# Optimization experiments

Measured on AMD Instinct MI355X. Metric: run time of the kernel, lower is better.

The kernel has to match this reference:

```python
import jax, jax.numpy as jnp
import numpy as np

# B trajectories, L spline knots, D data channels, H hidden, W MLP width, OUT outputs
B, L, D, H, W, OUT = 1024, 200, 32, 64, 128, 16
N_STEPS = 100  # dt0 = (ts[-1]-ts[0]) / 100 in the source -> fixed-step Heun over the span


def _mlp3(x, W1, b1, W2, b2, W3, b3, act, final_act=None):
    h = act(x @ W1.T + b1)
    h = act(h @ W2.T + b2)
    o = h @ W3.T + b3
    return final_act(o) if final_act is not None else o


def setup_inputs() -> dict:
    key = jax.random.key(0)
    ks = jax.random.split(key, 16)
    f32 = jnp.float32

    def rn(k, shape, scale):
        return jax.random.normal(k, shape, f32) * scale

    def lin(kk, out_d, in_d):
        kw, kb = jax.random.split(kk)
        s = 1.0 / float(np.sqrt(in_d))
        return rn(kw, (out_d, in_d), s), rn(kb, (out_d,), s)

    inp = {"ts": jnp.arange(L, dtype=f32)}
    for i, n in enumerate(["coef_d", "coef_c", "coef_b", "coef_a"]):
        inp[n] = rn(ks[i], (B, L - 1, D), 0.1)
    inp["iW1"], inp["ib1"] = lin(ks[4], W, D)
    inp["iW2"], inp["ib2"] = lin(ks[5], W, W)
    inp["iW3"], inp["ib3"] = lin(ks[6], H, W)
    inp["fW1"], inp["fb1"] = lin(ks[7], W, H)
    inp["fW2"], inp["fb2"] = lin(ks[8], W, W)
    inp["fW3"], inp["fb3"] = lin(ks[9], H * D, W)
    inp["dW1"], inp["db1"] = lin(ks[10], 128, H)
    inp["dW2"], inp["db2"] = lin(ks[11], 128, 128)
    inp["dW3"], inp["db3"] = lin(ks[12], OUT, 128)
    return inp


def reference(ts, coef_d, coef_c, coef_b, coef_a,
              iW1, ib1, iW2, ib2, iW3, ib3,
              fW1, fb1, fW2, fb2, fW3, fb3,
              dW1, db1, dW2, db2, dW3, db3):
    sp = jax.nn.softplus
    # X(t0) = a[:, 0] (cubic-spline eval at left knot has frac = 0)
    y0 = _mlp3(coef_a[:, 0], iW1, ib1, iW2, ib2, iW3, ib3, sp, final_act=sp)  # [B, H]
    t0 = ts[0]
    dt = (ts[-1] - t0) / N_STEPS

    def dXdt(t):  # cubic spline derivative at scalar time t -> [B, D]
        i = jnp.clip(jnp.searchsorted(ts, t, side="right") - 1, 0, L - 2)
        frac = t - ts[i]
        return coef_b[:, i] + frac * (2.0 * coef_c[:, i] + 3.0 * frac * coef_d[:, i])

    def vf(t, y):  # ControlTerm(func, control).to_ode(): f(y) @ dX/dt
        f = _mlp3(y, fW1, fb1, fW2, fb2, fW3, fb3, sp).reshape(B, H, D)
        return jnp.einsum("bhd,bd->bh", f, dXdt(t))

    def heun_step(y, k):
        t = t0 + k * dt
        k1 = vf(t, y)
        k2 = vf(t + dt, y + dt * k1)
        return y + 0.5 * dt * (k1 + k2), None

    yT, _ = jax.lax.scan(heun_step, y0, jnp.arange(N_STEPS, dtype=ts.dtype))
    # decoder: Linear->relu->Linear->relu->Linear
    return _mlp3(yT, dW1, db1, dW2, db2, dW3, db3, jax.nn.relu)  # [B, OUT]
```

## Files before the change

### kernel.cpp

```cpp
#include <hip/hip_runtime.h>

#define NT 512
#define TRAJ 4

constexpr int Lk = 200;
constexpr int NSTEPS = 100;

__device__ __forceinline__ float sp_act(float x) {
    return fmaxf(x, 0.0f) + log1pf(expf(-fabsf(x)));
}

__global__ void fw3_transpose(const float* __restrict__ w, float* __restrict__ wT) {
    int idx = blockIdx.x * 256 + threadIdx.x;
    int k = idx >> 11;
    int n = idx & 2047;
    wT[idx] = w[n * 128 + k];
}

template<int O, int I>
__device__ __forceinline__ void stage_T(const float* __restrict__ g, float* __restrict__ T) {
    for (int base = threadIdx.x * 4; base < O * I; base += NT * 4) {
        const float4 w = *(const float4*)(g + base);
        const int o = base / I;
        const int i = base % I;
        T[(i + 0) * O + o] = w.x;
        T[(i + 1) * O + o] = w.y;
        T[(i + 2) * O + o] = w.z;
        T[(i + 3) * O + o] = w.w;
    }
}

template<int I, int O, int ACT>
__device__ __forceinline__ void mlp_layer(const float* __restrict__ T,
                                          const float* __restrict__ bias,
                                          const float* __restrict__ in, int inStride,
                                          float* __restrict__ out, int outStride) {
    const int tid = threadIdx.x;
    constexpr int TOT = TRAJ * O;
    for (int e = tid; e < TOT; e += NT) {
        const int t = e / O;
        const int o = e % O;
        const float* inr = in + t * inStride;
        float acc = bias[o];
        #pragma unroll 4
        for (int i = 0; i < I; ++i) acc = fmaf(inr[i], T[i * O + o], acc);
        if (ACT == 1) acc = sp_act(acc);
        else if (ACT == 2) acc = fmaxf(acc, 0.0f);
        out[t * outStride + o] = acc;
    }
}

__device__ __forceinline__ void evalvf(float t,
                                       const float* __restrict__ yin,
                                       float* __restrict__ kout,
                                       const float* __restrict__ wT1,
                                       const float* __restrict__ wT2,
                                       const float* __restrict__ fb1s,
                                       const float* __restrict__ fb2s,
                                       float* __restrict__ h1s,
                                       float* __restrict__ h2s,
                                       float* __restrict__ dXs,
                                       const float* __restrict__ ts,
                                       const float* __restrict__ coef_b,
                                       const float* __restrict__ coef_c,
                                       const float* __restrict__ coef_d,
                                       int bbase,
                                       const float4* __restrict__ wp,
                                       float4 fb3r)
{
    const int tid = threadIdx.x;

    if (tid < TRAJ * 32) {
        int i = (int)floorf(t);
        i = min(max(i, 0), Lk - 2);
        const float frac = t - ts[i];
        const int tt = tid >> 5, d = tid & 31;
        const size_t off = ((size_t)(bbase + tt) * 199 + (size_t)i) * 32 + d;
        dXs[tid] = coef_b[off] + frac * (2.0f * coef_c[off] + 3.0f * frac * coef_d[off]);
    }
    mlp_layer<64, 128, 1>(wT1, fb1s, yin, 64, h1s, 128);
    __syncthreads();
    mlp_layer<128, 128, 1>(wT2, fb2s, h1s, 128, h2s, 128);
    __syncthreads();

    float4 acc[TRAJ];
    #pragma unroll
    for (int t4 = 0; t4 < TRAJ; ++t4) acc[t4] = make_float4(0.f, 0.f, 0.f, 0.f);

    for (int k0 = 0; k0 < 128; k0 += 4) {
        const float4 w0 = wp[(k0 + 0) * 512];
        const float4 w1 = wp[(k0 + 1) * 512];
        const float4 w2 = wp[(k0 + 2) * 512];
        const float4 w3 = wp[(k0 + 3) * 512];
        #pragma unroll
        for (int t4 = 0; t4 < TRAJ; ++t4) {
            const float4 h = *(const float4*)(h2s + t4 * 128 + k0);
            float4 a = acc[t4];
            a.x = fmaf(h.x, w0.x, a.x); a.y = fmaf(h.x, w0.y, a.y); a.z = fmaf(h.x, w0.z, a.z); a.w = fmaf(h.x, w0.w, a.w);
            a.x = fmaf(h.y, w1.x, a.x); a.y = fmaf(h.y, w1.y, a.y); a.z = fmaf(h.y, w1.z, a.z); a.w = fmaf(h.y, w1.w, a.w);
            a.x = fmaf(h.z, w2.x, a.x); a.y = fmaf(h.z, w2.y, a.y); a.z = fmaf(h.z, w2.z, a.z); a.w = fmaf(h.z, w2.w, a.w);
            a.x = fmaf(h.w, w3.x, a.x); a.y = fmaf(h.w, w3.y, a.y); a.z = fmaf(h.w, w3.z, a.z); a.w = fmaf(h.w, w3.w, a.w);
            acc[t4] = a;
        }
    }

    const int dbase = 4 * (tid & 7);
    float part[TRAJ];
    #pragma unroll
    for (int t4 = 0; t4 < TRAJ; ++t4) {
        const float4 dx = *(const float4*)(dXs + t4 * 32 + dbase);
        part[t4] = (acc[t4].x + fb3r.x) * dx.x + (acc[t4].y + fb3r.y) * dx.y +
                   (acc[t4].z + fb3r.z) * dx.z + (acc[t4].w + fb3r.w) * dx.w;
    }
    #pragma unroll
    for (int m = 1; m < 8; m <<= 1) {
        #pragma unroll
        for (int t4 = 0; t4 < TRAJ; ++t4) part[t4] += __shfl_xor(part[t4], m, 64);
    }
    if ((tid & 7) == 0) {
        const int h = tid >> 3;
        #pragma unroll
        for (int t4 = 0; t4 < TRAJ; ++t4) kout[t4 * 64 + h] = part[t4];
    }
    __syncthreads();
}

__global__ __launch_bounds__(NT, 1)
void cde_kernel(const float* __restrict__ ts,
                const float* __restrict__ coef_d, const float* __restrict__ coef_c,
                const float* __restrict__ coef_b, const float* __restrict__ coef_a,
                const float* __restrict__ iW1, const float* __restrict__ ib1,
                const float* __restrict__ iW2, const float* __restrict__ ib2,
                const float* __restrict__ iW3, const float* __restrict__ ib3,
                const float* __restrict__ fW1, const float* __restrict__ fb1,
                const float* __restrict__ fW2, const float* __restrict__ fb2,
                const float* __restrict__ fb3,
                const float* __restrict__ dW1, const float* __restrict__ db1,
                const float* __restrict__ dW2, const float* __restrict__ db2,
                const float* __restrict__ dW3, const float* __restrict__ db3,
                const float* __restrict__ fW3T,
                float* __restrict__ outp)
{
    __shared__ float wreg[28672];
    __shared__ float h1s[TRAJ * 128], h2s[TRAJ * 128];
    __shared__ float ys[TRAJ * 64], ys2[TRAJ * 64], k1s[TRAJ * 64], k2s[TRAJ * 64];
    __shared__ float dXs[TRAJ * 32], a0s[TRAJ * 32];
    __shared__ float fb1s[128], fb2s[128];

    const int tid = threadIdx.x;
    const int bbase = blockIdx.x * TRAJ;

    const float ts0 = ts[0];
    const float dt = (ts[Lk - 1] - ts0) / (float)NSTEPS;
    const float4 fb3r = *((const float4*)fb3 + tid);
    const float4* wp = (const float4*)fW3T + tid;

    if (tid < TRAJ * 32) {
        const int t = tid >> 5, d = tid & 31;
        a0s[t * 32 + d] = coef_a[((size_t)(bbase + t) * 199) * 32 + d];
    }
    stage_T<128, 32>(iW1, wreg);
    stage_T<128, 128>(iW2, wreg + 32 * 128);
    stage_T<64, 128>(iW3, wreg + 32 * 128 + 128 * 128);
    if (tid < 128) { fb1s[tid] = fb1[tid]; fb2s[tid] = fb2[tid]; }
    __syncthreads();
    mlp_layer<32, 128, 1>(wreg, ib1, a0s, 32, h1s, 128);
    __syncthreads();
    mlp_layer<128, 128, 1>(wreg + 32 * 128, ib2, h1s, 128, h2s, 128);
    __syncthreads();
    mlp_layer<128, 64, 1>(wreg + 32 * 128 + 128 * 128, ib3, h2s, 128, ys, 64);
    __syncthreads();

    stage_T<128, 64>(fW1, wreg);
    stage_T<128, 128>(fW2, wreg + 64 * 128);
    __syncthreads();

    for (int step = 0; step < NSTEPS; ++step) {
        const float t1 = ts0 + (float)step * dt;
        evalvf(t1, ys, k1s, wreg, wreg + 64 * 128, fb1s, fb2s, h1s, h2s, dXs,
               ts, coef_b, coef_c, coef_d, bbase, wp, fb3r);
        if (tid < TRAJ * 64) ys2[tid] = ys[tid] + dt * k1s[tid];
        __syncthreads();
        evalvf(t1 + dt, ys2, k2s, wreg, wreg + 64 * 128, fb1s, fb2s, h1s, h2s, dXs,
               ts, coef_b, coef_c, coef_d, bbase, wp, fb3r);
        if (tid < TRAJ * 64) ys[tid] += 0.5f * dt * (k1s[tid] + k2s[tid]);
        __syncthreads();
    }

    stage_T<128, 64>(dW1, wreg);
    stage_T<128, 128>(dW2, wreg + 64 * 128);
    stage_T<16, 128>(dW3, wreg + 64 * 128 + 128 * 128);
    __syncthreads();
    mlp_layer<64, 128, 2>(wreg, db1, ys, 64, h1s, 128);
    __syncthreads();
    mlp_layer<128, 128, 2>(wreg + 64 * 128, db2, h1s, 128, h2s, 128);
    __syncthreads();
    mlp_layer<128, 16, 0>(wreg + 64 * 128 + 128 * 128, db3, h2s, 128,
                          outp + (size_t)bbase * 16, 16);
}

extern "C" void kernel_launch(void* const* d_in, const int* in_sizes, int n_in,
                              void* d_out, int out_size, void* d_ws, size_t ws_size,
                              hipStream_t stream) {
    (void)in_sizes; (void)n_in; (void)out_size; (void)ws_size;
    const float* ts     = (const float*)d_in[0];
    const float* coef_d = (const float*)d_in[1];
    const float* coef_c = (const float*)d_in[2];
    const float* coef_b = (const float*)d_in[3];
    const float* coef_a = (const float*)d_in[4];
    const float* iW1 = (const float*)d_in[5];  const float* ib1 = (const float*)d_in[6];
    const float* iW2 = (const float*)d_in[7];  const float* ib2 = (const float*)d_in[8];
    const float* iW3 = (const float*)d_in[9];  const float* ib3 = (const float*)d_in[10];
    const float* fW1 = (const float*)d_in[11]; const float* fb1 = (const float*)d_in[12];
    const float* fW2 = (const float*)d_in[13]; const float* fb2 = (const float*)d_in[14];
    const float* fW3 = (const float*)d_in[15]; const float* fb3 = (const float*)d_in[16];
    const float* dW1 = (const float*)d_in[17]; const float* db1 = (const float*)d_in[18];
    const float* dW2 = (const float*)d_in[19]; const float* db2 = (const float*)d_in[20];
    const float* dW3 = (const float*)d_in[21]; const float* db3 = (const float*)d_in[22];

    float* fW3T = (float*)d_ws;

    fw3_transpose<<<1024, 256, 0, stream>>>(fW3, fW3T);
    cde_kernel<<<256, NT, 0, stream>>>(ts, coef_d, coef_c, coef_b, coef_a,
                                       iW1, ib1, iW2, ib2, iW3, ib3,
                                       fW1, fb1, fW2, fb2, fb3,
                                       dW1, db1, dW2, db2, dW3, db3,
                                       fW3T, (float*)d_out);
}
```

Baseline: 2.685 ms.

## Store fW3 as packed fp16 pairs and prefetch weight chunks across layer computation

The 128x2048 final vector-field weight is repacked once into half2 pairs, halving the global/L2 traffic streamed by each thread every vector-field evaluation. Weight loads are software-pipelined: the first chunk is issued before the two shared-memory MLP layers and each next chunk is loaded while the current one is converted and accumulated. This adds conversion instructions and more registers, and introduces fp16 rounding of weights, which may affect accuracy over 200 evaluations.

```diff
diff --git a/kernel.cpp b/kernel.cpp
--- a/kernel.cpp
+++ b/kernel.cpp
@@ -1,4 +1,5 @@
 #include <hip/hip_runtime.h>
+#include <hip/hip_fp16.h>
 
 #define NT 512
 #define TRAJ 4
@@ -10,11 +11,18 @@
     return fmaxf(x, 0.0f) + log1pf(expf(-fabsf(x)));
 }
 
-__global__ void fw3_transpose(const float* __restrict__ w, float* __restrict__ wT) {
+__device__ __forceinline__ float2 cvt2(unsigned int u) {
+    union { unsigned int u; __half2 h; } x;
+    x.u = u;
+    return __half22float2(x.h);
+}
+
+__global__ void fw3_pack(const float* __restrict__ w, __half2* __restrict__ wP) {
     int idx = blockIdx.x * 256 + threadIdx.x;
-    int k = idx >> 11;
-    int n = idx & 2047;
-    wT[idx] = w[n * 128 + k];
+    int kp = idx >> 11;
+    int n  = idx & 2047;
+    const float2 v = *(const float2*)(w + n * 128 + 2 * kp);
+    wP[idx] = __halves2half2(__float2half_rn(v.x), __float2half_rn(v.y));
 }
 
 template<int O, int I>
@@ -65,7 +73,7 @@
                                        const float* __restrict__ coef_c,
                                        const float* __restrict__ coef_d,
                                        int bbase,
-                                       const float4* __restrict__ wp,
+                                       const uint4* __restrict__ wph,
                                        float4 fb3r)
 {
     const int tid = threadIdx.x;
@@ -78,6 +86,11 @@
         const size_t off = ((size_t)(bbase + tt) * 199 + (size_t)i) * 32 + d;
         dXs[tid] = coef_b[off] + frac * (2.0f * coef_c[off] + 3.0f * frac * coef_d[off]);
     }
+
+    uint4 cur[4], nxt[4];
+    #pragma unroll
+    for (int i = 0; i < 4; ++i) cur[i] = wph[i * 512];
+
     mlp_layer<64, 128, 1>(wT1, fb1s, yin, 64, h1s, 128);
     __syncthreads();
     mlp_layer<128, 128, 1>(wT2, fb2s, h1s, 128, h2s, 128);
@@ -87,21 +100,47 @@
     #pragma unroll
     for (int t4 = 0; t4 < TRAJ; ++t4) acc[t4] = make_float4(0.f, 0.f, 0.f, 0.f);
 
-    for (int k0 = 0; k0 < 128; k0 += 4) {
-        const float4 w0 = wp[(k0 + 0) * 512];
-        const float4 w1 = wp[(k0 + 1) * 512];
-        const float4 w2 = wp[(k0 + 2) * 512];
-        const float4 w3 = wp[(k0 + 3) * 512];
+    #pragma unroll 2
+    for (int c = 0; c < 16; ++c) {
+        if (c < 15) {
+            const uint4* p = wph + (4 * (c + 1)) * 512;
+            #pragma unroll
+            for (int i = 0; i < 4; ++i) nxt[i] = p[i * 512];
+        }
+        float2 wf[4][4];
+        #pragma unroll
+        for (int i = 0; i < 4; ++i) {
+            wf[i][0] = cvt2(cur[i].x); wf[i][1] = cvt2(cur[i].y);
+            wf[i][2] = cvt2(cur[i].z); wf[i][3] = cvt2(cur[i].w);
+        }
         #pragma unroll
         for (int t4 = 0; t4 < TRAJ; ++t4) {
-            const float4 h = *(const float4*)(h2s + t4 * 128 + k0);
+            const float4 ha = *(const float4*)(h2s + t4 * 128 + 8 * c);
+            const float4 hb = *(const float4*)(h2s + t4 * 128 + 8 * c + 4);
             float4 a = acc[t4];
-            a.x = fmaf(h.x, w0.x, a.x); a.y = fmaf(h.x, w0.y, a.y); a.z = fmaf(h.x, w0.z, a.z); a.w = fmaf(h.x, w0.w, a.w);
-            a.x = fmaf(h.y, w1.x, a.x); a.y = fmaf(h.y, w1.y, a.y); a.z = fmaf(h.y, w1.z, a.z); a.w = fmaf(h.y, w1.w, a.w);
-            a.x = fmaf(h.z, w2.x, a.x); a.y = fmaf(h.z, w2.y, a.y); a.z = fmaf(h.z, w2.z, a.z); a.w = fmaf(h.z, w2.w, a.w);
-            a.x = fmaf(h.w, w3.x, a.x); a.y = fmaf(h.w, w3.y, a.y); a.z = fmaf(h.w, w3.z, a.z); a.w = fmaf(h.w, w3.w, a.w);
+            a.x = fmaf(wf[0][0].x, ha.x, a.x); a.x = fmaf(wf[0][0].y, ha.y, a.x);
+            a.y = fmaf(wf[0][1].x, ha.x, a.y); a.y = fmaf(wf[0][1].y, ha.y, a.y);
+            a.z = fmaf(wf[0][2].x, ha.x, a.z); a.z = fmaf(wf[0][2].y, ha.y, a.z);
+            a.w = fmaf(wf[0][3].x, ha.x, a.w); a.w = fmaf(wf[0][3].y, ha.y, a.w);
+
+            a.x = fmaf(wf[1][0].x, ha.z, a.x); a.x = fmaf(wf[1][0].y, ha.w, a.x);
+            a.y = fmaf(wf[1][1].x, ha.z, a.y); a.y = fmaf(wf[1][1].y, ha.w, a.y);
+            a.z = fmaf(wf[1][2].x, ha.z, a.z); a.z = fmaf(wf[1][2].y, ha.w, a.z);
+            a.w = fmaf(wf[1][3].x, ha.z, a.w); a.w = fmaf(wf[1][3].y, ha.w, a.w);
+
+            a.x = fmaf(wf[2][0].x, hb.x, a.x); a.x = fmaf(wf[2][0].y, hb.y, a.x);
+            a.y = fmaf(wf[2][1].x, hb.x, a.y); a.y = fmaf(wf[2][1].y, hb.y, a.y);
+            a.z = fmaf(wf[2][2].x, hb.x, a.z); a.z = fmaf(wf[2][2].y, hb.y, a.z);
+            a.w = fmaf(wf[2][3].x, hb.x, a.w); a.w = fmaf(wf[2][3].y, hb.y, a.w);
+
+            a.x = fmaf(wf[3][0].x, hb.z, a.x); a.x = fmaf(wf[3][0].y, hb.w, a.x);
+            a.y = fmaf(wf[3][1].x, hb.z, a.y); a.y = fmaf(wf[3][1].y, hb.w, a.y);
+            a.z = fmaf(wf[3][2].x, hb.z, a.z); a.z = fmaf(wf[3][2].y, hb.w, a.z);
+            a.w = fmaf(wf[3][3].x, hb.z, a.w); a.w = fmaf(wf[3][3].y, hb.w, a.w);
             acc[t4] = a;
         }
+        #pragma unroll
+        for (int i = 0; i < 4; ++i) cur[i] = nxt[i];
     }
 
     const int dbase = 4 * (tid & 7);
@@ -138,7 +177,7 @@
                 const float* __restrict__ dW1, const float* __restrict__ db1,
                 const float* __restrict__ dW2, const float* __restrict__ db2,
                 const float* __restrict__ dW3, const float* __restrict__ db3,
-                const float* __restrict__ fW3T,
+                const __half2* __restrict__ fW3P,
                 float* __restrict__ outp)
 {
     __shared__ float wreg[28672];
@@ -153,7 +192,7 @@
     const float ts0 = ts[0];
     const float dt = (ts[Lk - 1] - ts0) / (float)NSTEPS;
     const float4 fb3r = *((const float4*)fb3 + tid);
-    const float4* wp = (const float4*)fW3T + tid;
+    const uint4* wph = (const uint4*)fW3P + tid;
 
     if (tid < TRAJ * 32) {
         const int t = tid >> 5, d = tid & 31;
@@ -178,11 +217,11 @@
     for (int step = 0; step < NSTEPS; ++step) {
         const float t1 = ts0 + (float)step * dt;
         evalvf(t1, ys, k1s, wreg, wreg + 64 * 128, fb1s, fb2s, h1s, h2s, dXs,
-               ts, coef_b, coef_c, coef_d, bbase, wp, fb3r);
+               ts, coef_b, coef_c, coef_d, bbase, wph, fb3r);
         if (tid < TRAJ * 64) ys2[tid] = ys[tid] + dt * k1s[tid];
         __syncthreads();
         evalvf(t1 + dt, ys2, k2s, wreg, wreg + 64 * 128, fb1s, fb2s, h1s, h2s, dXs,
-               ts, coef_b, coef_c, coef_d, bbase, wp, fb3r);
+               ts, coef_b, coef_c, coef_d, bbase, wph, fb3r);
         if (tid < TRAJ * 64) ys[tid] += 0.5f * dt * (k1s[tid] + k2s[tid]);
         __syncthreads();
     }
@@ -218,12 +257,12 @@
     const float* dW2 = (const float*)d_in[19]; const float* db2 = (const float*)d_in[20];
     const float* dW3 = (const float*)d_in[21]; const float* db3 = (const float*)d_in[22];
 
-    float* fW3T = (float*)d_ws;
-
-    fw3_transpose<<<1024, 256, 0, stream>>>(fW3, fW3T);
+    __half2* fW3P = (__half2*)d_ws;
+
+    fw3_pack<<<512, 256, 0, stream>>>(fW3, fW3P);
     cde_kernel<<<256, NT, 0, stream>>>(ts, coef_d, coef_c, coef_b, coef_a,
                                        iW1, ib1, iW2, ib2, iW3, ib3,
                                        fW1, fb1, fW2, fb2, fb3,
                                        dW1, db1, dW2, db2, dW3, db3,
-                                       fW3T, (float*)d_out);
-}
+                                       fW3P, (float*)d_out);
+}
```

After: 2.782 ms. 1.04x slower.
